# Performance work log

Measured on AMD Instinct MI355X. Metric: run time of the kernel, lower is better.

Reference implementation:

```python
import jax, jax.numpy as jnp
import numpy as np

# NVFP4 (e2m1) 4-bit codebook: sign bit in the high position of the nibble
_NVFP4_CODE = jnp.array([0.0, 0.5, 1.0, 1.5, 2.0, 3.0, 4.0, 6.0,
                         -0.0, -0.5, -1.0, -1.5, -2.0, -3.0, -4.0, -6.0],
                        dtype=jnp.float32)

M = 4096          # tokens (batch*seq)
K = 4096          # in_features
N_NVFP4 = 2048
N_FP8 = 1024
N_FP16 = 1024
N = N_NVFP4 + N_FP8 + N_FP16  # out_features
BLOCK = 16        # NVFP4 scale block size along K


def setup_inputs() -> dict:
    key = jax.random.key(0)
    ks = jax.random.split(key, 8)
    x = jax.random.normal(ks[0], (M, K), dtype=jnp.float32)
    nvfp4_idx = jax.random.randint(ks[1], (N_NVFP4, K), 0, 16, dtype=jnp.int32)
    nvfp4_scales = jax.random.uniform(ks[2], (N_NVFP4, K // BLOCK), dtype=jnp.float32) * 0.5 + 0.05
    nvfp4_global_scale = jax.random.uniform(ks[3], (1,), dtype=jnp.float32) * 0.5 + 0.5
    w_fp8 = jax.random.normal(ks[4], (N_FP8, K), dtype=jnp.float32)
    fp8_scale = jax.random.uniform(ks[5], (1,), dtype=jnp.float32) * 0.1 + 0.01
    w_fp16 = jax.random.normal(ks[6], (N_FP16, K), dtype=jnp.float32) * 0.02
    bias = jax.random.normal(ks[7], (N,), dtype=jnp.float32) * 0.01
    inv_perm = jax.random.permutation(jax.random.fold_in(key, 99), N).astype(jnp.int64)
    return {"x": x, "nvfp4_idx": nvfp4_idx, "nvfp4_scales": nvfp4_scales,
            "nvfp4_global_scale": nvfp4_global_scale, "w_fp8": w_fp8,
            "fp8_scale": fp8_scale, "w_fp16": w_fp16, "bias": bias,
            "inv_perm": inv_perm}


def reference(x, nvfp4_idx, nvfp4_scales, nvfp4_global_scale,
              w_fp8, fp8_scale, w_fp16, bias, inv_perm):
    # --- NVFP4 group: dequantize 4-bit codes with per-16-block fp8 scales + global scale
    codes = _NVFP4_CODE[nvfp4_idx]                                   # [n_nvfp4, K]
    scales_full = jnp.repeat(nvfp4_scales, BLOCK, axis=1)            # [n_nvfp4, K]
    w_nvfp4 = codes * scales_full * nvfp4_global_scale[0]            # [n_nvfp4, K]
    y_nvfp4 = jnp.einsum('mk,nk->mn', x, w_nvfp4)                    # [M, n_nvfp4]
    # --- FP8 group: per-tensor scale
    y_fp8 = jnp.einsum('mk,nk->mn', x, w_fp8) * fp8_scale[0]         # [M, n_fp8]
    # --- FP16 group: plain GEMM
    y_fp16 = jnp.einsum('mk,nk->mn', x, w_fp16)                      # [M, n_fp16]
    # --- Reassemble in original channel order via inverse permutation
    y_grouped = jnp.concatenate([y_nvfp4, y_fp8, y_fp16], axis=-1)   # [M, N]
    y = jnp.take(y_grouped, inv_perm, axis=-1)
    return y + bias
```

## Files before the change

kernel.cpp:

```cpp
#include <hip/hip_runtime.h>

#define M_DIM 4096
#define N_DIM 4096
#define K_DIM 4096

typedef float f32x4 __attribute__((ext_vector_type(4)));
typedef __bf16 bf16x8 __attribute__((ext_vector_type(8)));

__device__ __forceinline__ unsigned short f2b(float f) {
    unsigned int u = __float_as_uint(f);
    u += 0x7fffu + ((u >> 16) & 1u);
    return (unsigned short)(u >> 16);
}

__device__ __forceinline__ float nvfp4_decode(int n) {
    unsigned m = (unsigned)n & 7u;
    unsigned e = m >> 1, f = m & 1u;
    unsigned bits = (m >= 2u) ? (((126u + e) << 23) | (f << 22))
                              : (m * 0x3f000000u);
    bits |= ((unsigned)n & 8u) << 28;
    return __uint_as_float(bits);
}

__global__ __launch_bounds__(256) void xconv_kernel(
        const float* __restrict__ x, unsigned short* __restrict__ xb) {
    size_t i = ((size_t)blockIdx.x * 256 + threadIdx.x) * 8;
    float4 a0 = *(const float4*)(x + i);
    float4 a1 = *(const float4*)(x + i + 4);
    union { unsigned short h[8]; uint4 u; } o;
    o.h[0] = f2b(a0.x); o.h[1] = f2b(a0.y); o.h[2] = f2b(a0.z); o.h[3] = f2b(a0.w);
    o.h[4] = f2b(a1.x); o.h[5] = f2b(a1.y); o.h[6] = f2b(a1.z); o.h[7] = f2b(a1.w);
    *(uint4*)(xb + i) = o.u;
}

__global__ __launch_bounds__(256) void wbuild_kernel(
        const int* __restrict__ idx4, const float* __restrict__ sc4,
        const float* __restrict__ gs4, const float* __restrict__ w8,
        const float* __restrict__ s8, const float* __restrict__ w16,
        const int* __restrict__ iperm, unsigned short* __restrict__ W) {
    const int j = blockIdx.x;
    const int t = threadIdx.x;
    const int g = iperm[j];

#pragma unroll
    for (int h = 0; h < 2; ++h) {
        const int k0 = h * 2048 + t * 8;
        union { unsigned short hh[8]; uint4 u; } o;
        if (g < 2048) {
            const float s = sc4[(size_t)g * (K_DIM / 16) + (k0 >> 4)] * gs4[0];
            const int4* ip = (const int4*)(idx4 + (size_t)g * K_DIM + k0);
            int4 v0 = ip[0], v1 = ip[1];
            o.hh[0] = f2b(nvfp4_decode(v0.x) * s);
            o.hh[1] = f2b(nvfp4_decode(v0.y) * s);
            o.hh[2] = f2b(nvfp4_decode(v0.z) * s);
            o.hh[3] = f2b(nvfp4_decode(v0.w) * s);
            o.hh[4] = f2b(nvfp4_decode(v1.x) * s);
            o.hh[5] = f2b(nvfp4_decode(v1.y) * s);
            o.hh[6] = f2b(nvfp4_decode(v1.z) * s);
            o.hh[7] = f2b(nvfp4_decode(v1.w) * s);
        } else if (g < 3072) {
            const float s = s8[0];
            const float4* wp = (const float4*)(w8 + (size_t)(g - 2048) * K_DIM + k0);
            float4 v0 = wp[0], v1 = wp[1];
            o.hh[0] = f2b(v0.x * s); o.hh[1] = f2b(v0.y * s);
            o.hh[2] = f2b(v0.z * s); o.hh[3] = f2b(v0.w * s);
            o.hh[4] = f2b(v1.x * s); o.hh[5] = f2b(v1.y * s);
            o.hh[6] = f2b(v1.z * s); o.hh[7] = f2b(v1.w * s);
        } else {
            const float4* wp = (const float4*)(w16 + (size_t)(g - 3072) * K_DIM + k0);
            float4 v0 = wp[0], v1 = wp[1];
            o.hh[0] = f2b(v0.x); o.hh[1] = f2b(v0.y);
            o.hh[2] = f2b(v0.z); o.hh[3] = f2b(v0.w);
            o.hh[4] = f2b(v1.x); o.hh[5] = f2b(v1.y);
            o.hh[6] = f2b(v1.z); o.hh[7] = f2b(v1.w);
        }
        *(uint4*)(W + (size_t)j * K_DIM + k0) = o.u;
    }
}

#define GLOAD_LDS16(g, l)                                                     \
    __builtin_amdgcn_global_load_lds(                                         \
        (const __attribute__((address_space(1))) void*)(unsigned long long)(g),\
        (__attribute__((address_space(3))) void*)(unsigned int)(unsigned long long)(l), \
        16, 0, 0)

#define STAGE(p, d, kt, buf) do {                                             \
    const unsigned short* _s = (p) + (size_t)(kt) * 64;                       \
    GLOAD_LDS16(_s,      smem + (buf) * 32768 + (d));                         \
    GLOAD_LDS16(_s + 32, smem + (buf) * 32768 + (d) + 1024);                  \
} while (0)

#define LOAD_A(buf, qm) do {                                                  \
    _Pragma("unroll") for (int mi = 0; mi < 4; ++mi)                          \
        _Pragma("unroll") for (int kk = 0; kk < 2; ++kk)                      \
            af[mi][kk] = *(const bf16x8*)(rdA + (buf) * 32768 +               \
                                          (((qm) * 8 + mi * 2 + kk) << 10));  \
} while (0)

#define LOAD_B(buf, qn) do {                                                  \
    _Pragma("unroll") for (int nj = 0; nj < 2; ++nj)                          \
        _Pragma("unroll") for (int kk = 0; kk < 2; ++kk)                      \
            bq[nj][kk] = *(const bf16x8*)(rdB + (buf) * 32768 +               \
                                          (((qn) * 4 + nj * 2 + kk) << 10));  \
} while (0)

#define MMA(qm, qn) do {                                                      \
    _Pragma("unroll") for (int mi = 0; mi < 4; ++mi)                          \
        _Pragma("unroll") for (int nj = 0; nj < 2; ++nj) {                    \
            acc[(qm)*4+mi][(qn)*2+nj] = __builtin_amdgcn_mfma_f32_16x16x32_bf16( \
                af[mi][0], bq[nj][0], acc[(qm)*4+mi][(qn)*2+nj], 0, 0, 0);    \
            acc[(qm)*4+mi][(qn)*2+nj] = __builtin_amdgcn_mfma_f32_16x16x32_bf16( \
                af[mi][1], bq[nj][1], acc[(qm)*4+mi][(qn)*2+nj], 0, 0, 0);    \
        }                                                                     \
} while (0)

#define BARRIER __builtin_amdgcn_s_barrier()
#define WAIT_LGKM asm volatile("s_waitcnt lgkmcnt(0)" ::: "memory")
#define WAIT_VM4 asm volatile("s_waitcnt vmcnt(4)" ::: "memory")
#define PRIO1 __builtin_amdgcn_s_setprio(1)
#define PRIO0 __builtin_amdgcn_s_setprio(0)

__global__ __launch_bounds__(512, 2) void gemm_kernel(
        const unsigned short* __restrict__ X, const unsigned short* __restrict__ W,
        const float* __restrict__ bias, float* __restrict__ C) {
    __shared__ __align__(128) unsigned char smem[131072];

    const int pid = blockIdx.x;
    const int wg = (pid & 7) * 32 + (pid >> 3);
    const int bm = wg >> 4, bn = wg & 15;
    const int m0 = bm * 256, n0 = bn * 256;

    const int tid  = threadIdx.x;
    const int wave = tid >> 6;
    const int lane = tid & 63;
    const int wr   = wave >> 2;
    const int wc   = wave & 3;
    const int l16  = lane & 15;
    const int quad = lane >> 4;

    const int srow = lane >> 2;
    const int scol = ((lane & 3) ^ ((lane >> 5) << 1)) << 3;

    const unsigned short* pA0 = X + (size_t)(m0 + (wr * 8 + wc) * 16 + srow) * K_DIM + scol;
    const unsigned short* pA1 = pA0 + (size_t)64 * K_DIM;
    const unsigned short* pB0 = W + (size_t)(n0 + (wc * 4 + wr) * 16 + srow) * K_DIM + scol;
    const unsigned short* pB1 = pB0 + (size_t)32 * K_DIM;

    const int dA0 = (((wr * 8 + wc) * 2) << 10) + lane * 16;
    const int dA1 = dA0 + 8192;
    const int dB0 = 65536 + (((wc * 4 + wr) * 2) << 10) + lane * 16;
    const int dB1 = dB0 + 4096;

    const int inner_rd = ((l16 << 6) | (quad << 4)) ^ ((l16 & 8) << 2);
    const unsigned char* rdA = smem + ((wr * 16) << 10) + inner_rd;
    const unsigned char* rdB = smem + 65536 + ((wc * 8) << 10) + inner_rd;

    f32x4 acc[8][4] = {};
    bf16x8 af[4][2], bq[2][2];

    STAGE(pA0, dA0, 0, 0);
    STAGE(pB0, dB0, 0, 0);
    STAGE(pB1, dB1, 0, 0);
    STAGE(pA1, dA1, 0, 0);
    STAGE(pA0, dA0, 1, 1);
    STAGE(pB1, dB1, 1, 1);
    WAIT_VM4;
    BARRIER;

#pragma unroll 1
    for (int it = 0; it < 32; ++it) {
        const int t1 = 2 * it + 1;
        const int t2 = (2 * it + 2) & 63;
        const int t3 = (2 * it + 3) & 63;

        LOAD_A(0, 0); LOAD_B(0, 0);
        STAGE(pB0, dB0, t1, 1);
        BARRIER; WAIT_LGKM;
        PRIO1; MMA(0, 0); PRIO0;
        BARRIER;
        LOAD_B(0, 1);
        STAGE(pA1, dA1, t1, 1);
        BARRIER; WAIT_LGKM;
        PRIO1; MMA(0, 1); PRIO0;
        BARRIER;
        LOAD_A(0, 1);
        STAGE(pA0, dA0, t2, 0);
        BARRIER; WAIT_LGKM;
        PRIO1; MMA(1, 1); PRIO0;
        BARRIER;
        LOAD_B(0, 0);
        STAGE(pB1, dB1, t2, 0);
        BARRIER; WAIT_LGKM;
        PRIO1; MMA(1, 0); PRIO0;
        WAIT_VM4;
        BARRIER;

        LOAD_A(1, 0); LOAD_B(1, 0);
        STAGE(pB0, dB0, t2, 0);
        BARRIER; WAIT_LGKM;
        PRIO1; MMA(0, 0); PRIO0;
        BARRIER;
        LOAD_B(1, 1);
        STAGE(pA1, dA1, t2, 0);
        BARRIER; WAIT_LGKM;
        PRIO1; MMA(0, 1); PRIO0;
        BARRIER;
        LOAD_A(1, 1);
        STAGE(pA0, dA0, t3, 1);
        BARRIER; WAIT_LGKM;
        PRIO1; MMA(1, 1); PRIO0;
        BARRIER;
        LOAD_B(1, 0);
        STAGE(pB1, dB1, t3, 1);
        BARRIER; WAIT_LGKM;
        PRIO1; MMA(1, 0); PRIO0;
        WAIT_VM4;
        BARRIER;
    }

    const int crow0 = m0 + wr * 128 + quad * 4;
    const int ccol0 = n0 + wc * 64 + l16;
    float bv[4];
#pragma unroll
    for (int p = 0; p < 4; ++p) bv[p] = bias[ccol0 + p * 16];
#pragma unroll
    for (int q = 0; q < 8; ++q) {
#pragma unroll
        for (int p = 0; p < 4; ++p) {
            const int col = ccol0 + p * 16;
            const int row = crow0 + q * 16;
#pragma unroll
            for (int r = 0; r < 4; ++r)
                C[(size_t)(row + r) * N_DIM + col] = acc[q][p][r] + bv[p];
        }
    }
}

extern "C" void kernel_launch(void* const* d_in, const int* in_sizes, int n_in,
                              void* d_out, int out_size, void* d_ws, size_t ws_size,
                              hipStream_t stream) {
    const float* x            = (const float*)d_in[0];
    const int*   nvfp4_idx    = (const int*)d_in[1];
    const float* nvfp4_scales = (const float*)d_in[2];
    const float* gscale       = (const float*)d_in[3];
    const float* w_fp8        = (const float*)d_in[4];
    const float* fp8_scale    = (const float*)d_in[5];
    const float* w_fp16       = (const float*)d_in[6];
    const float* bias         = (const float*)d_in[7];
    const int*   inv_perm     = (const int*)d_in[8];
    float* out = (float*)d_out;

    unsigned short* xb = (unsigned short*)d_ws;
    unsigned short* wb = xb + (size_t)M_DIM * K_DIM;

    xconv_kernel<<<8192, 256, 0, stream>>>(x, xb);
    wbuild_kernel<<<4096, 256, 0, stream>>>(nvfp4_idx, nvfp4_scales, gscale,
                                            w_fp8, fp8_scale, w_fp16,
                                            inv_perm, wb);
    gemm_kernel<<<(M_DIM / 256) * (N_DIM / 256), 512, 0, stream>>>(xb, wb, bias, out);
}
```

Baseline: 295.8 us.

## Fuse prep and GEMM into one cooperative kernel and reorder MFMA quadrant schedule

The two preprocessing kernels (x to bf16, and weight dequant plus permute) and the GEMM are merged into a single cooperative launch of 256 blocks, separated by a grid-wide sync. If the cooperative launch fails, it falls back to a separate prep kernel and GEMM kernel. The GEMM inner loop now keeps two A-fragment register sets so the fourth quadrant reuses already-loaded A and B fragments, which drops one LDS load phase and its wait. This removes launch gaps and some LDS traffic, but the prep work now runs on only 256 blocks of 512 threads and adds a grid barrier and extra registers.

Result: slower. 362.3 us (+22.5%).

```diff
diff --git a/kernel.cpp b/kernel.cpp
--- a/kernel.cpp
+++ b/kernel.cpp
@@ -1,4 +1,7 @@
 #include <hip/hip_runtime.h>
+#include <hip/hip_cooperative_groups.h>
+
+namespace cg = cooperative_groups;
 
 #define M_DIM 4096
 #define N_DIM 4096
@@ -22,32 +25,36 @@
     return __uint_as_float(bits);
 }
 
-__global__ __launch_bounds__(256) void xconv_kernel(
-        const float* __restrict__ x, unsigned short* __restrict__ xb) {
-    size_t i = ((size_t)blockIdx.x * 256 + threadIdx.x) * 8;
-    float4 a0 = *(const float4*)(x + i);
-    float4 a1 = *(const float4*)(x + i + 4);
-    union { unsigned short h[8]; uint4 u; } o;
-    o.h[0] = f2b(a0.x); o.h[1] = f2b(a0.y); o.h[2] = f2b(a0.z); o.h[3] = f2b(a0.w);
-    o.h[4] = f2b(a1.x); o.h[5] = f2b(a1.y); o.h[6] = f2b(a1.z); o.h[7] = f2b(a1.w);
-    *(uint4*)(xb + i) = o.u;
-}
-
-__global__ __launch_bounds__(256) void wbuild_kernel(
+__device__ __forceinline__ void prep_body(
+        const float* __restrict__ x, unsigned short* __restrict__ xb,
         const int* __restrict__ idx4, const float* __restrict__ sc4,
         const float* __restrict__ gs4, const float* __restrict__ w8,
         const float* __restrict__ s8, const float* __restrict__ w16,
         const int* __restrict__ iperm, unsigned short* __restrict__ W) {
-    const int j = blockIdx.x;
+    const int b = blockIdx.x;
     const int t = threadIdx.x;
-    const int g = iperm[j];
-
-#pragma unroll
-    for (int h = 0; h < 2; ++h) {
-        const int k0 = h * 2048 + t * 8;
+
+#pragma unroll 4
+    for (int i = 0; i < 16; ++i) {
+        const size_t off = ((size_t)(b * 16 + i) * 512 + t) * 8;
+        float4 a0 = *(const float4*)(x + off);
+        float4 a1 = *(const float4*)(x + off + 4);
+        union { unsigned short h[8]; uint4 u; } o;
+        o.h[0] = f2b(a0.x); o.h[1] = f2b(a0.y); o.h[2] = f2b(a0.z); o.h[3] = f2b(a0.w);
+        o.h[4] = f2b(a1.x); o.h[5] = f2b(a1.y); o.h[6] = f2b(a1.z); o.h[7] = f2b(a1.w);
+        *(uint4*)(xb + off) = o.u;
+    }
+
+    const float gs = gs4[0];
+    const float s8v = s8[0];
+#pragma unroll 2
+    for (int i = 0; i < 16; ++i) {
+        const int j = b * 16 + i;
+        const int g = iperm[j];
+        const int k0 = t * 8;
         union { unsigned short hh[8]; uint4 u; } o;
         if (g < 2048) {
-            const float s = sc4[(size_t)g * (K_DIM / 16) + (k0 >> 4)] * gs4[0];
+            const float s = sc4[(size_t)g * (K_DIM / 16) + (k0 >> 4)] * gs;
             const int4* ip = (const int4*)(idx4 + (size_t)g * K_DIM + k0);
             int4 v0 = ip[0], v1 = ip[1];
             o.hh[0] = f2b(nvfp4_decode(v0.x) * s);
@@ -59,13 +66,12 @@
             o.hh[6] = f2b(nvfp4_decode(v1.z) * s);
             o.hh[7] = f2b(nvfp4_decode(v1.w) * s);
         } else if (g < 3072) {
-            const float s = s8[0];
             const float4* wp = (const float4*)(w8 + (size_t)(g - 2048) * K_DIM + k0);
             float4 v0 = wp[0], v1 = wp[1];
-            o.hh[0] = f2b(v0.x * s); o.hh[1] = f2b(v0.y * s);
-            o.hh[2] = f2b(v0.z * s); o.hh[3] = f2b(v0.w * s);
-            o.hh[4] = f2b(v1.x * s); o.hh[5] = f2b(v1.y * s);
-            o.hh[6] = f2b(v1.z * s); o.hh[7] = f2b(v1.w * s);
+            o.hh[0] = f2b(v0.x * s8v); o.hh[1] = f2b(v0.y * s8v);
+            o.hh[2] = f2b(v0.z * s8v); o.hh[3] = f2b(v0.w * s8v);
+            o.hh[4] = f2b(v1.x * s8v); o.hh[5] = f2b(v1.y * s8v);
+            o.hh[6] = f2b(v1.z * s8v); o.hh[7] = f2b(v1.w * s8v);
         } else {
             const float4* wp = (const float4*)(w16 + (size_t)(g - 3072) * K_DIM + k0);
             float4 v0 = wp[0], v1 = wp[1];
@@ -90,27 +96,27 @@
     GLOAD_LDS16(_s + 32, smem + (buf) * 32768 + (d) + 1024);                  \
 } while (0)
 
-#define LOAD_A(buf, qm) do {                                                  \
+#define LOADA(AF, buf, qm) do {                                               \
     _Pragma("unroll") for (int mi = 0; mi < 4; ++mi)                          \
         _Pragma("unroll") for (int kk = 0; kk < 2; ++kk)                      \
-            af[mi][kk] = *(const bf16x8*)(rdA + (buf) * 32768 +               \
+            AF[mi][kk] = *(const bf16x8*)(rdA + (buf) * 32768 +               \
                                           (((qm) * 8 + mi * 2 + kk) << 10));  \
 } while (0)
 
-#define LOAD_B(buf, qn) do {                                                  \
+#define LOADB(buf, qn) do {                                                   \
     _Pragma("unroll") for (int nj = 0; nj < 2; ++nj)                          \
         _Pragma("unroll") for (int kk = 0; kk < 2; ++kk)                      \
             bq[nj][kk] = *(const bf16x8*)(rdB + (buf) * 32768 +               \
                                           (((qn) * 4 + nj * 2 + kk) << 10));  \
 } while (0)
 
-#define MMA(qm, qn) do {                                                      \
+#define MMA(AF, qm, qn) do {                                                  \
     _Pragma("unroll") for (int mi = 0; mi < 4; ++mi)                          \
         _Pragma("unroll") for (int nj = 0; nj < 2; ++nj) {                    \
             acc[(qm)*4+mi][(qn)*2+nj] = __builtin_amdgcn_mfma_f32_16x16x32_bf16( \
-                af[mi][0], bq[nj][0], acc[(qm)*4+mi][(qn)*2+nj], 0, 0, 0);    \
+                AF[mi][0], bq[nj][0], acc[(qm)*4+mi][(qn)*2+nj], 0, 0, 0);    \
             acc[(qm)*4+mi][(qn)*2+nj] = __builtin_amdgcn_mfma_f32_16x16x32_bf16( \
-                af[mi][1], bq[nj][1], acc[(qm)*4+mi][(qn)*2+nj], 0, 0, 0);    \
+                AF[mi][1], bq[nj][1], acc[(qm)*4+mi][(qn)*2+nj], 0, 0, 0);    \
         }                                                                     \
 } while (0)
 
@@ -120,7 +126,7 @@
 #define PRIO1 __builtin_amdgcn_s_setprio(1)
 #define PRIO0 __builtin_amdgcn_s_setprio(0)
 
-__global__ __launch_bounds__(512, 2) void gemm_kernel(
+__device__ __forceinline__ void gemm_body(
         const unsigned short* __restrict__ X, const unsigned short* __restrict__ W,
         const float* __restrict__ bias, float* __restrict__ C) {
     __shared__ __align__(128) unsigned char smem[131072];
@@ -156,7 +162,7 @@
     const unsigned char* rdB = smem + 65536 + ((wc * 8) << 10) + inner_rd;
 
     f32x4 acc[8][4] = {};
-    bf16x8 af[4][2], bq[2][2];
+    bf16x8 af0[4][2], af1[4][2], bq[2][2];
 
     STAGE(pA0, dA0, 0, 0);
     STAGE(pB0, dB0, 0, 0);
@@ -173,47 +179,45 @@
         const int t2 = (2 * it + 2) & 63;
         const int t3 = (2 * it + 3) & 63;
 
-        LOAD_A(0, 0); LOAD_B(0, 0);
+        LOADA(af0, 0, 0); LOADB(0, 0);
         STAGE(pB0, dB0, t1, 1);
         BARRIER; WAIT_LGKM;
-        PRIO1; MMA(0, 0); PRIO0;
-        BARRIER;
-        LOAD_B(0, 1);
+        PRIO1; MMA(af0, 0, 0); PRIO0;
+        BARRIER;
+        LOADA(af1, 0, 1);
         STAGE(pA1, dA1, t1, 1);
         BARRIER; WAIT_LGKM;
-        PRIO1; MMA(0, 1); PRIO0;
-        BARRIER;
-        LOAD_A(0, 1);
+        PRIO1; MMA(af1, 1, 0); PRIO0;
+        BARRIER;
+        LOADB(0, 1);
         STAGE(pA0, dA0, t2, 0);
         BARRIER; WAIT_LGKM;
-        PRIO1; MMA(1, 1); PRIO0;
-        BARRIER;
-        LOAD_B(0, 0);
+        PRIO1; MMA(af1, 1, 1); PRIO0;
+        BARRIER;
         STAGE(pB1, dB1, t2, 0);
-        BARRIER; WAIT_LGKM;
-        PRIO1; MMA(1, 0); PRIO0;
+        BARRIER;
+        PRIO1; MMA(af0, 0, 1); PRIO0;
         WAIT_VM4;
         BARRIER;
 
-        LOAD_A(1, 0); LOAD_B(1, 0);
+        LOADA(af0, 1, 0); LOADB(1, 0);
         STAGE(pB0, dB0, t2, 0);
         BARRIER; WAIT_LGKM;
-        PRIO1; MMA(0, 0); PRIO0;
-        BARRIER;
-        LOAD_B(1, 1);
+        PRIO1; MMA(af0, 0, 0); PRIO0;
+        BARRIER;
+        LOADA(af1, 1, 1);
         STAGE(pA1, dA1, t2, 0);
         BARRIER; WAIT_LGKM;
-        PRIO1; MMA(0, 1); PRIO0;
-        BARRIER;
-        LOAD_A(1, 1);
+        PRIO1; MMA(af1, 1, 0); PRIO0;
+        BARRIER;
+        LOADB(1, 1);
         STAGE(pA0, dA0, t3, 1);
         BARRIER; WAIT_LGKM;
-        PRIO1; MMA(1, 1); PRIO0;
-        BARRIER;
-        LOAD_B(1, 0);
+        PRIO1; MMA(af1, 1, 1); PRIO0;
+        BARRIER;
         STAGE(pB1, dB1, t3, 1);
-        BARRIER; WAIT_LGKM;
-        PRIO1; MMA(1, 0); PRIO0;
+        BARRIER;
+        PRIO1; MMA(af0, 0, 1); PRIO0;
         WAIT_VM4;
         BARRIER;
     }
@@ -234,6 +238,33 @@
                 C[(size_t)(row + r) * N_DIM + col] = acc[q][p][r] + bv[p];
         }
     }
+}
+
+__global__ __launch_bounds__(512, 2) void fused_kernel(
+        const float* __restrict__ x, unsigned short* __restrict__ xb,
+        const int* __restrict__ idx4, const float* __restrict__ sc4,
+        const float* __restrict__ gs4, const float* __restrict__ w8,
+        const float* __restrict__ s8, const float* __restrict__ w16,
+        const int* __restrict__ iperm, unsigned short* __restrict__ wb,
+        const float* __restrict__ bias, float* __restrict__ out) {
+    prep_body(x, xb, idx4, sc4, gs4, w8, s8, w16, iperm, wb);
+    cg::this_grid().sync();
+    gemm_body(xb, wb, bias, out);
+}
+
+__global__ __launch_bounds__(512, 2) void prep_kernel(
+        const float* __restrict__ x, unsigned short* __restrict__ xb,
+        const int* __restrict__ idx4, const float* __restrict__ sc4,
+        const float* __restrict__ gs4, const float* __restrict__ w8,
+        const float* __restrict__ s8, const float* __restrict__ w16,
+        const int* __restrict__ iperm, unsigned short* __restrict__ wb) {
+    prep_body(x, xb, idx4, sc4, gs4, w8, s8, w16, iperm, wb);
+}
+
+__global__ __launch_bounds__(512, 2) void gemm_kernel(
+        const unsigned short* __restrict__ X, const unsigned short* __restrict__ W,
+        const float* __restrict__ bias, float* __restrict__ C) {
+    gemm_body(X, W, bias, C);
 }
 
 extern "C" void kernel_launch(void* const* d_in, const int* in_sizes, int n_in,
@@ -253,9 +284,15 @@
     unsigned short* xb = (unsigned short*)d_ws;
     unsigned short* wb = xb + (size_t)M_DIM * K_DIM;
 
-    xconv_kernel<<<8192, 256, 0, stream>>>(x, xb);
-    wbuild_kernel<<<4096, 256, 0, stream>>>(nvfp4_idx, nvfp4_scales, gscale,
-                                            w_fp8, fp8_scale, w_fp16,
-                                            inv_perm, wb);
-    gemm_kernel<<<(M_DIM / 256) * (N_DIM / 256), 512, 0, stream>>>(xb, wb, bias, out);
-}
+    void* fargs[] = {(void*)&x, (void*)&xb, (void*)&nvfp4_idx, (void*)&nvfp4_scales,
+                     (void*)&gscale, (void*)&w_fp8, (void*)&fp8_scale, (void*)&w_fp16,
+                     (void*)&inv_perm, (void*)&wb, (void*)&bias, (void*)&out};
+    hipError_t e = hipLaunchCooperativeKernel((const void*)fused_kernel,
+                                              dim3(256), dim3(512), fargs, 0, stream);
+    if (e != hipSuccess) {
+        prep_kernel<<<256, 512, 0, stream>>>(x, xb, nvfp4_idx, nvfp4_scales,
+                                             gscale, w_fp8, fp8_scale, w_fp16,
+                                             inv_perm, wb);
+        gemm_kernel<<<256, 512, 0, stream>>>(xb, wb, bias, out);
+    }
+}
```
